# Kernel optimization log

Hardware: AMD Instinct MI355X
Metric: run time of the kernel (lower is better)

Reference implementation:

```python
import jax, jax.numpy as jnp
import numpy as np

B, L, D_MODEL, HEADS, EXP, DEPTH = 2, 2048, 1024, 16, 2, 12
D_EXP = D_MODEL * EXP
D_HEAD = D_EXP // HEADS


def _layernorm(x, g, b, eps=1e-5):
    mu = jnp.mean(x, axis=-1, keepdims=True)
    var = jnp.mean(jnp.square(x - mu), axis=-1, keepdims=True)
    return (x - mu) * jax.lax.rsqrt(var + eps) * g + b


def setup_inputs() -> dict:
    key = jax.random.key(0)
    ks = jax.random.split(key, 4)
    x = jax.random.normal(ks[0], (B, L, D_MODEL), dtype=jnp.float32)
    w_in = jax.random.normal(ks[1], (D_MODEL, 4 * D_EXP), dtype=jnp.float32) * 0.02
    w_out = jax.random.normal(ks[2], (D_EXP, D_MODEL), dtype=jnp.float32) * (0.02 / np.sqrt(2 * DEPTH))
    return {
        "x": x,
        "ln1_g": jnp.ones((D_MODEL,), jnp.float32),
        "ln1_b": jnp.zeros((D_MODEL,), jnp.float32),
        "ln2_g": jnp.ones((D_MODEL,), jnp.float32),
        "ln2_b": jnp.zeros((D_MODEL,), jnp.float32),
        "w_in": w_in,
        "w_out": w_out,
        "smear_factor": jnp.linspace(-6.0, 6.0, HEADS, dtype=jnp.float32),
        "log_scale": jnp.zeros((HEADS,), jnp.float32),
    }


def reference(x, ln1_g, ln1_b, ln2_g, ln2_b, w_in, w_out, smear_factor, log_scale):
    b, l, d = x.shape
    h = smear_factor.shape[0]
    d_exp = w_in.shape[1] // 4
    dh = d_exp // h

    qkvp = _layernorm(x, ln1_g, ln1_b) @ w_in  # [b, l, 4*d_exp]
    q, k, v, p = jnp.split(qkvp, 4, axis=-1)
    # 'b i (h d) -> b h i d'
    to_heads = lambda t: t.reshape(b, l, h, dh).transpose(0, 2, 1, 3)
    q, k, v = to_heads(q), to_heads(k), to_heads(v)

    # smeared keys: k_i <- (1-s)*k_i + s*k_{i-1}  (zero at i=0)
    smear = jax.nn.sigmoid(smear_factor)[None, :, None, None]
    k_prev = jnp.pad(k, ((0, 0), (0, 0), (1, 0), (0, 0)))[:, :, :-1, :]
    k = (1.0 - smear) * k + smear * k_prev

    # ALiBi-style additive mask: slope[h]*j on causal part, -1e10 above diag
    half = h // 2
    slopes = jnp.concatenate([2.0 ** jnp.linspace(0.0, -8.0, half), jnp.zeros((h - half,), jnp.float32)])
    j = jnp.arange(l)
    causal = jnp.where(j[None, :] > j[:, None], jnp.float32(-1e10), jnp.float32(0.0))  # [l, l]
    mask = slopes[:, None, None] * j[None, None, :].astype(jnp.float32) + causal[None, :, :]  # [h, l, l]

    # SDPA with q/s, k/s and default scale 1/sqrt(dh): logits = q k^T / (s^2 sqrt(dh))
    inv = 1.0 / (jnp.exp(2.0 * log_scale)[None, :, None, None] * jnp.sqrt(jnp.float32(dh)))
    logits = jnp.einsum('bhid,bhjd->bhij', q, k) * inv + mask[None]
    attn = jax.nn.softmax(logits, axis=-1)
    o = jnp.einsum('bhij,bhjd->bhid', attn, v)
    o = o.transpose(0, 2, 1, 3).reshape(b, l, h * dh)  # 'b h i d -> b i (h d)'

    out = (jax.nn.silu(p) * o) @ w_out
    return _layernorm(out, ln2_g, ln2_b)
```

## Files before the change

kernel.cpp:

```cpp
#include <hip/hip_runtime.h>

typedef unsigned short u16;
typedef __attribute__((ext_vector_type(8))) short bf16x8;
typedef __attribute__((ext_vector_type(8))) unsigned short u16x8;
typedef __attribute__((ext_vector_type(4))) float f32x4;

#define L_SEQ 2048
#define NTOK 4096
#define DMODEL 1024
#define DEXP 2048
#define NH 16
#define DH 128

__device__ __forceinline__ u16 f2bf(float f) {
    unsigned u = __float_as_uint(f);
    unsigned r = (u + 0x7FFFu + ((u >> 16) & 1u)) >> 16;
    return (u16)r;
}
__device__ __forceinline__ float bf2f(u16 h) {
    return __uint_as_float(((unsigned)h) << 16);
}

template <int CTRL>
__device__ __forceinline__ float dpp_f(float x) {
    return __int_as_float(__builtin_amdgcn_update_dpp(0, __float_as_int(x), CTRL, 0xF, 0xF, true));
}
__device__ __forceinline__ float red16_max(float x) {
    x = fmaxf(x, dpp_f<0xB1>(x));
    x = fmaxf(x, dpp_f<0x4E>(x));
    x = fmaxf(x, dpp_f<0x124>(x));
    x = fmaxf(x, dpp_f<0x128>(x));
    return x;
}
__device__ __forceinline__ float red16_sum(float x) {
    x += dpp_f<0xB1>(x);
    x += dpp_f<0x4E>(x);
    x += dpp_f<0x124>(x);
    x += dpp_f<0x128>(x);
    return x;
}

__device__ __forceinline__ void gl_lds16(const u16* g, u16* l) {
    __builtin_amdgcn_global_load_lds((const __attribute__((address_space(1))) void*)g,
                                     (__attribute__((address_space(3))) void*)l, 16, 0, 0);
}

__global__ void conv_transpose(const float* __restrict__ in, u16* __restrict__ out, int R, int C) {
    __shared__ unsigned tile[32][33];
    int c0 = blockIdx.x * 32, r0 = blockIdx.y * 32;
    int tx = threadIdx.x, ty = threadIdx.y;
    for (int j = 0; j < 32; j += 8)
        tile[ty + j][tx] = (unsigned)f2bf(in[(size_t)(r0 + ty + j) * C + c0 + tx]);
    __syncthreads();
    for (int j = 0; j < 32; j += 8)
        out[(size_t)(c0 + ty + j) * R + r0 + tx] = (u16)tile[tx][ty + j];
}

__global__ __launch_bounds__(256) void ln_fwd(const float* __restrict__ x, const float* __restrict__ g,
                                              const float* __restrict__ bta, void* __restrict__ outp,
                                              int out_bf16) {
    int row = blockIdx.x;
    int t = threadIdx.x;
    const float* xr = x + (size_t)row * DMODEL;
    float4 xv = *(const float4*)&xr[t * 4];
    float s = xv.x + xv.y + xv.z + xv.w;
    float s2 = xv.x * xv.x + xv.y * xv.y + xv.z * xv.z + xv.w * xv.w;
    for (int off = 32; off >= 1; off >>= 1) {
        s += __shfl_xor(s, off);
        s2 += __shfl_xor(s2, off);
    }
    __shared__ float red[10];
    int w = t >> 6;
    if ((t & 63) == 0) { red[w] = s; red[4 + w] = s2; }
    __syncthreads();
    if (t == 0) {
        red[8] = red[0] + red[1] + red[2] + red[3];
        red[9] = red[4] + red[5] + red[6] + red[7];
    }
    __syncthreads();
    float mu = red[8] * (1.0f / DMODEL);
    float var = red[9] * (1.0f / DMODEL) - mu * mu;
    float rstd = rsqrtf(var + 1e-5f);
    float vals[4] = {xv.x, xv.y, xv.z, xv.w};
    for (int e = 0; e < 4; e++) {
        int c = t * 4 + e;
        float y = (vals[e] - mu) * rstd * g[c] + bta[c];
        if (out_bf16) ((u16*)outp)[(size_t)row * DMODEL + c] = f2bf(y);
        else          ((float*)outp)[(size_t)row * DMODEL + c] = y;
    }
}

__device__ __forceinline__ void store_out(u16* C, size_t idx, float v) { C[idx] = f2bf(v); }
__device__ __forceinline__ void store_out(float* C, size_t idx, float v) { C[idx] = v; }

template <typename OutT>
__global__ __launch_bounds__(256) void gemm_bt(const u16* __restrict__ A, const u16* __restrict__ BT,
                                               OutT* __restrict__ C, int M, int N, int K) {
    __shared__ u16 a_s[4096];
    __shared__ u16 b_s[4096];
    int tid = threadIdx.x;
    int m0 = blockIdx.y * 128, n0 = blockIdx.x * 128;
    int w = tid >> 6, lane = tid & 63, quad = lane >> 4, ln = lane & 15;
    int wr = (w >> 1) * 64, wc = (w & 1) * 64;
    f32x4 zero4 = {0.f, 0.f, 0.f, 0.f};
    f32x4 acc[4][4];
    for (int r = 0; r < 4; r++)
        for (int c = 0; c < 4; c++) acc[r][c] = zero4;

    int lrow = lane >> 2, lseg = (lane & 3) * 8;
    const u16* Ag0 = A + (size_t)(m0 + 32 * w + lrow) * K + lseg;
    const u16* Ag1 = Ag0 + (size_t)16 * K;
    const u16* Bg0 = BT + (size_t)(n0 + 32 * w + lrow) * K + lseg;
    const u16* Bg1 = Bg0 + (size_t)16 * K;
    u16* al0 = &a_s[(2 * w) * 512];
    u16* al1 = &a_s[(2 * w + 1) * 512];
    u16* bl0 = &b_s[(2 * w) * 512];
    u16* bl1 = &b_s[(2 * w + 1) * 512];

    for (int k0 = 0; k0 < K; k0 += 32) {
        __syncthreads();
        gl_lds16(Ag0 + k0, al0);
        gl_lds16(Ag1 + k0, al1);
        gl_lds16(Bg0 + k0, bl0);
        gl_lds16(Bg1 + k0, bl1);
        __syncthreads();
        bf16x8 af[4], bfr[4];
        for (int r = 0; r < 4; r++) af[r]  = *(const bf16x8*)&a_s[(wr + r * 16 + ln) * 32 + quad * 8];
        for (int c = 0; c < 4; c++) bfr[c] = *(const bf16x8*)&b_s[(wc + c * 16 + ln) * 32 + quad * 8];
        for (int r = 0; r < 4; r++)
            for (int c = 0; c < 4; c++)
                acc[r][c] = __builtin_amdgcn_mfma_f32_16x16x32_bf16(af[r], bfr[c], acc[r][c], 0, 0, 0);
    }
    for (int r = 0; r < 4; r++)
        for (int c = 0; c < 4; c++)
            for (int e = 0; e < 4; e++) {
                int row = m0 + wr + r * 16 + quad * 4 + e;
                int col = n0 + wc + c * 16 + ln;
                store_out(C, (size_t)row * N + col, acc[r][c][e]);
            }
}

__global__ __launch_bounds__(256) void smear_kernel(const u16* __restrict__ qkvp,
                                                    const float* __restrict__ smear_f,
                                                    u16* __restrict__ k_sm) {
    int gid = blockIdx.x * 256 + threadIdx.x;
    int base = gid * 8;
    int bl = base >> 11;
    int c = base & 2047;
    int h = c >> 7;
    int d = c & 127;
    int l = bl & (L_SEQ - 1);
    int bb = bl >> 11;
    float s = 1.0f / (1.0f + __expf(-smear_f[h]));
    u16x8 cur = *(const u16x8*)&qkvp[(size_t)bl * 8192 + 2048 + c];
    u16x8 prv = {0, 0, 0, 0, 0, 0, 0, 0};
    if (l > 0) prv = *(const u16x8*)&qkvp[(size_t)(bl - 1) * 8192 + 2048 + c];
    u16x8 outv;
    for (int u = 0; u < 8; u++) {
        float kc = bf2f(cur[u]);
        float kp = bf2f(prv[u]);
        outv[u] = f2bf((1.0f - s) * kc + s * kp);
    }
    *(u16x8*)&k_sm[(((size_t)(bb * 16 + h)) * L_SEQ + l) * DH + d] = outv;
}

__global__ void vT_kernel(const u16* __restrict__ qkvp, u16* __restrict__ v_t) {
    __shared__ unsigned tile[32][33];
    int l0 = blockIdx.x * 32, d0 = blockIdx.y * 32;
    int bh = blockIdx.z;
    int bb = bh >> 4, h = bh & 15;
    int tx = threadIdx.x, ty = threadIdx.y;
    size_t tokb = (size_t)bb * L_SEQ;
    for (int j = 0; j < 32; j += 8)
        tile[ty + j][tx] = (unsigned)qkvp[(tokb + l0 + ty + j) * 8192 + 4096 + h * DH + d0 + tx];
    __syncthreads();
    for (int j = 0; j < 32; j += 8)
        v_t[((size_t)bh * DH + d0 + ty + j) * L_SEQ + l0 + tx] = (u16)tile[tx][ty + j];
}

__global__ __launch_bounds__(256) void attn_kernel(const u16* __restrict__ qkvp,
                                                   const u16* __restrict__ k_sm,
                                                   const u16* __restrict__ v_t,
                                                   u16* __restrict__ ag2,
                                                   const float* __restrict__ log_scale) {
    __shared__ u16 k_s[8192];
    __shared__ u16 vt_s[8192];
    __shared__ u16 p_s[4608];
    int tid = threadIdx.x;
    int bh = blockIdx.y;
    int bb = bh >> 4, h = bh & 15;
    int w = tid >> 6, lane = tid & 63, quad = lane >> 4, ln = lane & 15;
    size_t tokb = (size_t)bb * L_SEQ;

    const float LOG2E = 1.44269504f;
    float inv = 1.0f / (__expf(2.0f * log_scale[h]) * sqrtf((float)DH));
    float scl = inv * LOG2E;
    float slope2 = ((h < 8) ? exp2f(-8.0f * (float)h / 7.0f) : 0.0f) * LOG2E;

    int lrow = lane >> 2, lseg8 = (lane & 3) * 8;
    f32x4 zero4 = {0.f, 0.f, 0.f, 0.f};
    u16* pw = &p_s[w * 1152];

    for (int sidx = 0; sidx < 2; sidx++) {
        int ib = sidx == 0 ? (31 - (int)blockIdx.x) : (int)blockIdx.x;
        int i0 = ib * 64;
        int si = i0 + w * 16;

        bf16x8 qf[4];
        for (int kt = 0; kt < 4; kt++)
            qf[kt] = *(const bf16x8*)&qkvp[(tokb + si + ln) * 8192 + h * DH + kt * 32 + quad * 8];

        float m_i[4], l_i[4];
        for (int r = 0; r < 4; r++) { m_i[r] = -1e30f; l_i[r] = 0.f; }
        f32x4 o_acc[8];
        for (int dt = 0; dt < 8; dt++) o_acc[dt] = zero4;

        const u16* kg[4];
        for (int g = 0; g < 4; g++)
            kg[g] = k_sm + ((size_t)bh * L_SEQ + g * 16 + lrow) * DH + w * 32 + lseg8;
        const u16* vg[4];
        u16* vl[4];
        for (int q = 0; q < 4; q++) {
            int c = w * 4 + q;
            int jt = c >> 3, dg = c & 7;
            vg[q] = v_t + ((size_t)bh * DH + dg * 16 + lrow) * L_SEQ + jt * 32 + lseg8;
            vl[q] = &vt_s[jt * 4096 + dg * 512];
        }

        for (int j0 = 0; j0 <= i0; j0 += 64) {
            __syncthreads();
            for (int g = 0; g < 4; g++) {
                gl_lds16(kg[g], &k_s[w * 2048 + g * 512]);
                kg[g] += 64 * DH;
            }
            for (int q = 0; q < 4; q++) {
                gl_lds16(vg[q], vl[q]);
                vg[q] += 64;
            }
            __syncthreads();

            f32x4 sc[4];
            for (int ct = 0; ct < 4; ct++) sc[ct] = zero4;
            for (int kt = 0; kt < 4; kt++)
                for (int ct = 0; ct < 4; ct++) {
                    bf16x8 bfr = *(const bf16x8*)&k_s[kt * 2048 + (ct * 16 + ln) * 32 + quad * 8];
                    sc[ct] = __builtin_amdgcn_mfma_f32_16x16x32_bf16(qf[kt], bfr, sc[ct], 0, 0, 0);
                }

            bool full = (j0 + 63 <= si);
            float s2[4][4];
            float aj0 = slope2 * (float)(j0 + ln);
            for (int ct = 0; ct < 4; ct++) {
                float ajv = aj0 + slope2 * (float)(16 * ct);
                int j = j0 + ct * 16 + ln;
                for (int r = 0; r < 4; r++) {
                    float v = fmaf(sc[ct][r], scl, ajv);
                    if (!full) {
                        int i = si + quad * 4 + r;
                        if (j > i) v = -3.0e38f;
                    }
                    s2[ct][r] = v;
                }
            }
            float mnew[4], alpha[4];
            for (int r = 0; r < 4; r++) {
                float mr = fmaxf(fmaxf(s2[0][r], s2[1][r]), fmaxf(s2[2][r], s2[3][r]));
                mr = red16_max(mr);
                mnew[r] = fmaxf(m_i[r], mr);
                alpha[r] = exp2f(m_i[r] - mnew[r]);
                m_i[r] = mnew[r];
            }
            float rs[4] = {0.f, 0.f, 0.f, 0.f};
            for (int ct = 0; ct < 4; ct++)
                for (int r = 0; r < 4; r++) {
                    float p = exp2f(s2[ct][r] - mnew[r]);
                    u16 pb = (u16)(__float_as_uint(p) >> 16);
                    pw[(quad * 4 + r) * 72 + ct * 16 + ln] = pb;
                    rs[r] += bf2f(pb);
                }
            for (int r = 0; r < 4; r++) {
                float s = red16_sum(rs[r]);
                l_i[r] = fmaf(alpha[r], l_i[r], s);
            }
            for (int dt = 0; dt < 8; dt++) {
                f32x4 o = o_acc[dt];
                for (int r = 0; r < 4; r++) o[r] *= alpha[r];
                o_acc[dt] = o;
            }
            asm volatile("s_waitcnt lgkmcnt(0)" ::: "memory");
            for (int ks = 0; ks < 2; ks++) {
                bf16x8 pa = *(const bf16x8*)&pw[ln * 72 + ks * 32 + quad * 8];
                for (int dt = 0; dt < 8; dt++) {
                    bf16x8 vf = *(const bf16x8*)&vt_s[ks * 4096 + (dt * 16 + ln) * 32 + quad * 8];
                    o_acc[dt] = __builtin_amdgcn_mfma_f32_16x16x32_bf16(pa, vf, o_acc[dt], 0, 0, 0);
                }
            }
        }

        float rinv[4];
        for (int r = 0; r < 4; r++) rinv[r] = __builtin_amdgcn_rcpf(l_i[r]);
        for (int dt = 0; dt < 8; dt++)
            for (int r = 0; r < 4; r++) {
                int i = si + quad * 4 + r;
                int dcol = dt * 16 + ln;
                float o = o_acc[dt][r] * rinv[r];
                float pv = bf2f(qkvp[(tokb + i) * 8192 + 6144 + h * DH + dcol]);
                float gate = pv * __builtin_amdgcn_rcpf(1.0f + exp2f(-pv * LOG2E));
                ag2[(tokb + i) * 2048 + h * DH + dcol] = f2bf(gate * o);
            }
    }
}

extern "C" void kernel_launch(void* const* d_in, const int* in_sizes, int n_in,
                              void* d_out, int out_size, void* d_ws, size_t ws_size,
                              hipStream_t stream) {
    const float* x       = (const float*)d_in[0];
    const float* ln1_g   = (const float*)d_in[1];
    const float* ln1_b   = (const float*)d_in[2];
    const float* ln2_g   = (const float*)d_in[3];
    const float* ln2_b   = (const float*)d_in[4];
    const float* w_in    = (const float*)d_in[5];
    const float* w_out   = (const float*)d_in[6];
    const float* smear_f = (const float*)d_in[7];
    const float* logsc   = (const float*)d_in[8];
    float* out = (float*)d_out;
    char* ws = (char*)d_ws;

    u16* w_inT   = (u16*)(ws + 0);
    u16* w_outT  = (u16*)(ws + (size_t)16777216);
    u16* lnA     = (u16*)(ws + (size_t)20971520);
    u16* qkvp    = (u16*)(ws + (size_t)29360128);
    u16* k_sm    = (u16*)(ws + (size_t)96468992);
    u16* ag2     = (u16*)(ws + (size_t)113246208);
    float* out_pre = (float*)(ws + (size_t)96468992);
    u16* v_t     = (u16*)(ws + 0);

    dim3 b32x8(32, 8);
    conv_transpose<<<dim3(8192 / 32, 1024 / 32), b32x8, 0, stream>>>(w_in, w_inT, 1024, 8192);
    conv_transpose<<<dim3(1024 / 32, 2048 / 32), b32x8, 0, stream>>>(w_out, w_outT, 2048, 1024);
    ln_fwd<<<NTOK, 256, 0, stream>>>(x, ln1_g, ln1_b, (void*)lnA, 1);
    gemm_bt<u16><<<dim3(8192 / 128, 4096 / 128), 256, 0, stream>>>(lnA, w_inT, qkvp, NTOK, 8192, 1024);
    smear_kernel<<<4096, 256, 0, stream>>>(qkvp, smear_f, k_sm);
    vT_kernel<<<dim3(L_SEQ / 32, DH / 32, 32), b32x8, 0, stream>>>(qkvp, v_t);
    attn_kernel<<<dim3(16, 32), 256, 0, stream>>>(qkvp, k_sm, v_t, ag2, logsc);
    gemm_bt<float><<<dim3(1024 / 128, 4096 / 128), 256, 0, stream>>>(ag2, w_outT, out_pre, NTOK, 1024, 2048);
    ln_fwd<<<NTOK, 256, 0, stream>>>(out_pre, ln2_g, ln2_b, (void*)out, 0);
}
```

Baseline: 389.5 us.

## Enlarge attention query tile to 128 rows with MFMA row sums

Each attention block now handles one 128-row query tile, with each wave owning two 16-row m-tiles, so every K/V tile staged in LDS feeds twice as many MFMAs. This replaces the earlier scheme where each block processed two 64-row tiles paired for causal load balance. The softmax row sum is now accumulated with an MFMA against a ones vector instead of DPP reductions. Output rescaling is skipped when no row max changed, and launch bounds request two blocks per CU. The cost is that work per block is no longer balanced across the causal triangle, and register pressure rises from the doubled accumulators.

```diff
diff --git a/kernel.cpp b/kernel.cpp
--- a/kernel.cpp
+++ b/kernel.cpp
@@ -30,13 +30,6 @@
     x = fmaxf(x, dpp_f<0x4E>(x));
     x = fmaxf(x, dpp_f<0x124>(x));
     x = fmaxf(x, dpp_f<0x128>(x));
-    return x;
-}
-__device__ __forceinline__ float red16_sum(float x) {
-    x += dpp_f<0xB1>(x);
-    x += dpp_f<0x4E>(x);
-    x += dpp_f<0x124>(x);
-    x += dpp_f<0x128>(x);
     return x;
 }
 
@@ -178,132 +171,149 @@
         v_t[((size_t)bh * DH + d0 + ty + j) * L_SEQ + l0 + tx] = (u16)tile[tx][ty + j];
 }
 
-__global__ __launch_bounds__(256) void attn_kernel(const u16* __restrict__ qkvp,
-                                                   const u16* __restrict__ k_sm,
-                                                   const u16* __restrict__ v_t,
-                                                   u16* __restrict__ ag2,
-                                                   const float* __restrict__ log_scale) {
+__global__ __launch_bounds__(256, 2) void attn_kernel(const u16* __restrict__ qkvp,
+                                                      const u16* __restrict__ k_sm,
+                                                      const u16* __restrict__ v_t,
+                                                      u16* __restrict__ ag2,
+                                                      const float* __restrict__ log_scale) {
     __shared__ u16 k_s[8192];
     __shared__ u16 vt_s[8192];
-    __shared__ u16 p_s[4608];
+    __shared__ u16 p_s[9216];
     int tid = threadIdx.x;
+    int ib = 15 - (int)blockIdx.x;
+    int i0 = ib * 128;
     int bh = blockIdx.y;
     int bb = bh >> 4, h = bh & 15;
     int w = tid >> 6, lane = tid & 63, quad = lane >> 4, ln = lane & 15;
     size_t tokb = (size_t)bb * L_SEQ;
+    int si = i0 + w * 32;
 
     const float LOG2E = 1.44269504f;
     float inv = 1.0f / (__expf(2.0f * log_scale[h]) * sqrtf((float)DH));
     float scl = inv * LOG2E;
     float slope2 = ((h < 8) ? exp2f(-8.0f * (float)h / 7.0f) : 0.0f) * LOG2E;
 
+    bf16x8 qf[2][4];
+    for (int mt = 0; mt < 2; mt++)
+        for (int kt = 0; kt < 4; kt++)
+            qf[mt][kt] = *(const bf16x8*)&qkvp[(tokb + si + mt * 16 + ln) * 8192 + h * DH + kt * 32 + quad * 8];
+
+    float m_i[2][4];
+    for (int mt = 0; mt < 2; mt++)
+        for (int r = 0; r < 4; r++) m_i[mt][r] = -1e30f;
+    f32x4 zero4 = {0.f, 0.f, 0.f, 0.f};
+    f32x4 o_acc[2][8], l_acc[2];
+    for (int mt = 0; mt < 2; mt++) {
+        for (int dt = 0; dt < 8; dt++) o_acc[mt][dt] = zero4;
+        l_acc[mt] = zero4;
+    }
+    const short ONE_BF = (short)0x3F80;
+    bf16x8 ones = {ONE_BF, ONE_BF, ONE_BF, ONE_BF, ONE_BF, ONE_BF, ONE_BF, ONE_BF};
+
     int lrow = lane >> 2, lseg8 = (lane & 3) * 8;
-    f32x4 zero4 = {0.f, 0.f, 0.f, 0.f};
-    u16* pw = &p_s[w * 1152];
-
-    for (int sidx = 0; sidx < 2; sidx++) {
-        int ib = sidx == 0 ? (31 - (int)blockIdx.x) : (int)blockIdx.x;
-        int i0 = ib * 64;
-        int si = i0 + w * 16;
-
-        bf16x8 qf[4];
+    const u16* kg[4];
+    for (int g = 0; g < 4; g++)
+        kg[g] = k_sm + ((size_t)bh * L_SEQ + g * 16 + lrow) * DH + w * 32 + lseg8;
+    const u16* vg[4];
+    u16* vl[4];
+    for (int q = 0; q < 4; q++) {
+        int c = w * 4 + q;
+        int jt = c >> 3, dg = c & 7;
+        vg[q] = v_t + ((size_t)bh * DH + dg * 16 + lrow) * L_SEQ + jt * 32 + lseg8;
+        vl[q] = &vt_s[jt * 4096 + dg * 512];
+    }
+    u16* pw = &p_s[w * 2304];
+
+    for (int j0 = 0; j0 <= i0 + 64; j0 += 64) {
+        __syncthreads();
+        for (int g = 0; g < 4; g++) {
+            gl_lds16(kg[g], &k_s[w * 2048 + g * 512]);
+            kg[g] += 64 * DH;
+        }
+        for (int q = 0; q < 4; q++) {
+            gl_lds16(vg[q], vl[q]);
+            vg[q] += 64;
+        }
+        __syncthreads();
+        if (j0 > si + 31) continue;
+
+        f32x4 sc[2][4];
+        for (int mt = 0; mt < 2; mt++)
+            for (int ct = 0; ct < 4; ct++) sc[mt][ct] = zero4;
         for (int kt = 0; kt < 4; kt++)
-            qf[kt] = *(const bf16x8*)&qkvp[(tokb + si + ln) * 8192 + h * DH + kt * 32 + quad * 8];
-
-        float m_i[4], l_i[4];
-        for (int r = 0; r < 4; r++) { m_i[r] = -1e30f; l_i[r] = 0.f; }
-        f32x4 o_acc[8];
-        for (int dt = 0; dt < 8; dt++) o_acc[dt] = zero4;
-
-        const u16* kg[4];
-        for (int g = 0; g < 4; g++)
-            kg[g] = k_sm + ((size_t)bh * L_SEQ + g * 16 + lrow) * DH + w * 32 + lseg8;
-        const u16* vg[4];
-        u16* vl[4];
-        for (int q = 0; q < 4; q++) {
-            int c = w * 4 + q;
-            int jt = c >> 3, dg = c & 7;
-            vg[q] = v_t + ((size_t)bh * DH + dg * 16 + lrow) * L_SEQ + jt * 32 + lseg8;
-            vl[q] = &vt_s[jt * 4096 + dg * 512];
-        }
-
-        for (int j0 = 0; j0 <= i0; j0 += 64) {
-            __syncthreads();
-            for (int g = 0; g < 4; g++) {
-                gl_lds16(kg[g], &k_s[w * 2048 + g * 512]);
-                kg[g] += 64 * DH;
-            }
-            for (int q = 0; q < 4; q++) {
-                gl_lds16(vg[q], vl[q]);
-                vg[q] += 64;
-            }
-            __syncthreads();
-
-            f32x4 sc[4];
-            for (int ct = 0; ct < 4; ct++) sc[ct] = zero4;
-            for (int kt = 0; kt < 4; kt++)
-                for (int ct = 0; ct < 4; ct++) {
-                    bf16x8 bfr = *(const bf16x8*)&k_s[kt * 2048 + (ct * 16 + ln) * 32 + quad * 8];
-                    sc[ct] = __builtin_amdgcn_mfma_f32_16x16x32_bf16(qf[kt], bfr, sc[ct], 0, 0, 0);
-                }
-
-            bool full = (j0 + 63 <= si);
+            for (int ct = 0; ct < 4; ct++) {
+                bf16x8 bfr = *(const bf16x8*)&k_s[kt * 2048 + (ct * 16 + ln) * 32 + quad * 8];
+                sc[0][ct] = __builtin_amdgcn_mfma_f32_16x16x32_bf16(qf[0][kt], bfr, sc[0][ct], 0, 0, 0);
+                sc[1][ct] = __builtin_amdgcn_mfma_f32_16x16x32_bf16(qf[1][kt], bfr, sc[1][ct], 0, 0, 0);
+            }
+
+        float alpha[2][4];
+        bool any_resc = false;
+        float aj0 = slope2 * (float)(j0 + ln);
+        for (int mt = 0; mt < 2; mt++) {
+            int smt = si + mt * 16;
+            bool full = (j0 + 63 <= smt);
             float s2[4][4];
-            float aj0 = slope2 * (float)(j0 + ln);
             for (int ct = 0; ct < 4; ct++) {
                 float ajv = aj0 + slope2 * (float)(16 * ct);
                 int j = j0 + ct * 16 + ln;
                 for (int r = 0; r < 4; r++) {
-                    float v = fmaf(sc[ct][r], scl, ajv);
+                    float v = fmaf(sc[mt][ct][r], scl, ajv);
                     if (!full) {
-                        int i = si + quad * 4 + r;
+                        int i = smt + quad * 4 + r;
                         if (j > i) v = -3.0e38f;
                     }
                     s2[ct][r] = v;
                 }
             }
-            float mnew[4], alpha[4];
             for (int r = 0; r < 4; r++) {
                 float mr = fmaxf(fmaxf(s2[0][r], s2[1][r]), fmaxf(s2[2][r], s2[3][r]));
                 mr = red16_max(mr);
-                mnew[r] = fmaxf(m_i[r], mr);
-                alpha[r] = exp2f(m_i[r] - mnew[r]);
-                m_i[r] = mnew[r];
-            }
-            float rs[4] = {0.f, 0.f, 0.f, 0.f};
-            for (int ct = 0; ct < 4; ct++)
-                for (int r = 0; r < 4; r++) {
-                    float p = exp2f(s2[ct][r] - mnew[r]);
+                float mnew = fmaxf(m_i[mt][r], mr);
+                alpha[mt][r] = exp2f(m_i[mt][r] - mnew);
+                any_resc |= (alpha[mt][r] != 1.0f);
+                m_i[mt][r] = mnew;
+                for (int ct = 0; ct < 4; ct++) {
+                    float p = exp2f(s2[ct][r] - mnew);
                     u16 pb = (u16)(__float_as_uint(p) >> 16);
-                    pw[(quad * 4 + r) * 72 + ct * 16 + ln] = pb;
-                    rs[r] += bf2f(pb);
+                    pw[(mt * 16 + quad * 4 + r) * 72 + ct * 16 + ln] = pb;
                 }
-            for (int r = 0; r < 4; r++) {
-                float s = red16_sum(rs[r]);
-                l_i[r] = fmaf(alpha[r], l_i[r], s);
-            }
+            }
+        }
+        if (__any(any_resc)) {
+            for (int mt = 0; mt < 2; mt++) {
+                for (int dt = 0; dt < 8; dt++) {
+                    f32x4 o = o_acc[mt][dt];
+                    for (int r = 0; r < 4; r++) o[r] *= alpha[mt][r];
+                    o_acc[mt][dt] = o;
+                }
+                f32x4 lv = l_acc[mt];
+                for (int r = 0; r < 4; r++) lv[r] *= alpha[mt][r];
+                l_acc[mt] = lv;
+            }
+        }
+        asm volatile("s_waitcnt lgkmcnt(0)" ::: "memory");
+        for (int ks = 0; ks < 2; ks++) {
+            bf16x8 pa0 = *(const bf16x8*)&pw[ln * 72 + ks * 32 + quad * 8];
+            bf16x8 pa1 = *(const bf16x8*)&pw[(16 + ln) * 72 + ks * 32 + quad * 8];
+            l_acc[0] = __builtin_amdgcn_mfma_f32_16x16x32_bf16(pa0, ones, l_acc[0], 0, 0, 0);
+            l_acc[1] = __builtin_amdgcn_mfma_f32_16x16x32_bf16(pa1, ones, l_acc[1], 0, 0, 0);
             for (int dt = 0; dt < 8; dt++) {
-                f32x4 o = o_acc[dt];
-                for (int r = 0; r < 4; r++) o[r] *= alpha[r];
-                o_acc[dt] = o;
-            }
-            asm volatile("s_waitcnt lgkmcnt(0)" ::: "memory");
-            for (int ks = 0; ks < 2; ks++) {
-                bf16x8 pa = *(const bf16x8*)&pw[ln * 72 + ks * 32 + quad * 8];
-                for (int dt = 0; dt < 8; dt++) {
-                    bf16x8 vf = *(const bf16x8*)&vt_s[ks * 4096 + (dt * 16 + ln) * 32 + quad * 8];
-                    o_acc[dt] = __builtin_amdgcn_mfma_f32_16x16x32_bf16(pa, vf, o_acc[dt], 0, 0, 0);
-                }
-            }
-        }
-
+                bf16x8 vf = *(const bf16x8*)&vt_s[ks * 4096 + (dt * 16 + ln) * 32 + quad * 8];
+                o_acc[0][dt] = __builtin_amdgcn_mfma_f32_16x16x32_bf16(pa0, vf, o_acc[0][dt], 0, 0, 0);
+                o_acc[1][dt] = __builtin_amdgcn_mfma_f32_16x16x32_bf16(pa1, vf, o_acc[1][dt], 0, 0, 0);
+            }
+        }
+    }
+
+    for (int mt = 0; mt < 2; mt++) {
         float rinv[4];
-        for (int r = 0; r < 4; r++) rinv[r] = __builtin_amdgcn_rcpf(l_i[r]);
+        for (int r = 0; r < 4; r++) rinv[r] = __builtin_amdgcn_rcpf(l_acc[mt][r]);
         for (int dt = 0; dt < 8; dt++)
             for (int r = 0; r < 4; r++) {
-                int i = si + quad * 4 + r;
+                int i = si + mt * 16 + quad * 4 + r;
                 int dcol = dt * 16 + ln;
-                float o = o_acc[dt][r] * rinv[r];
+                float o = o_acc[mt][dt][r] * rinv[r];
                 float pv = bf2f(qkvp[(tokb + i) * 8192 + 6144 + h * DH + dcol]);
                 float gate = pv * __builtin_amdgcn_rcpf(1.0f + exp2f(-pv * LOG2E));
                 ag2[(tokb + i) * 2048 + h * DH + dcol] = f2bf(gate * o);
```

Result: slower. 413.4 us (+6.1%).

## Compute softmax row sums via MFMA with ones, skip masked tiles and rescales

Applied to the files above, without the earlier changes.

The per-row softmax denominator is no longer built from scalar adds plus DPP cross-lane reductions. It is accumulated with an extra MFMA that multiplies the P tile by a ones vector, using the bf16-rounded P values. Warps whose 16 rows lie entirely before the current key tile now skip score and PV work after the shared loads. The O and l rescale by alpha is skipped when no lane's running max changed. These changes cut VALU and cross-lane work in the attention inner loop, at the cost of one more MFMA per k-step and a wave-wide vote.

```diff
diff --git a/kernel.cpp b/kernel.cpp
--- a/kernel.cpp
+++ b/kernel.cpp
@@ -30,13 +30,6 @@
     x = fmaxf(x, dpp_f<0x4E>(x));
     x = fmaxf(x, dpp_f<0x124>(x));
     x = fmaxf(x, dpp_f<0x128>(x));
-    return x;
-}
-__device__ __forceinline__ float red16_sum(float x) {
-    x += dpp_f<0xB1>(x);
-    x += dpp_f<0x4E>(x);
-    x += dpp_f<0x124>(x);
-    x += dpp_f<0x128>(x);
     return x;
 }
 
@@ -200,6 +193,8 @@
     int lrow = lane >> 2, lseg8 = (lane & 3) * 8;
     f32x4 zero4 = {0.f, 0.f, 0.f, 0.f};
     u16* pw = &p_s[w * 1152];
+    const short ONE_BF = (short)0x3F80;
+    bf16x8 ones = {ONE_BF, ONE_BF, ONE_BF, ONE_BF, ONE_BF, ONE_BF, ONE_BF, ONE_BF};
 
     for (int sidx = 0; sidx < 2; sidx++) {
         int ib = sidx == 0 ? (31 - (int)blockIdx.x) : (int)blockIdx.x;
@@ -210,10 +205,11 @@
         for (int kt = 0; kt < 4; kt++)
             qf[kt] = *(const bf16x8*)&qkvp[(tokb + si + ln) * 8192 + h * DH + kt * 32 + quad * 8];
 
-        float m_i[4], l_i[4];
-        for (int r = 0; r < 4; r++) { m_i[r] = -1e30f; l_i[r] = 0.f; }
-        f32x4 o_acc[8];
+        float m_i[4];
+        for (int r = 0; r < 4; r++) m_i[r] = -1e30f;
+        f32x4 o_acc[8], l_acc;
         for (int dt = 0; dt < 8; dt++) o_acc[dt] = zero4;
+        l_acc = zero4;
 
         const u16* kg[4];
         for (int g = 0; g < 4; g++)
@@ -238,6 +234,7 @@
                 vg[q] += 64;
             }
             __syncthreads();
+            if (j0 > si + 15) continue;
 
             f32x4 sc[4];
             for (int ct = 0; ct < 4; ct++) sc[ct] = zero4;
@@ -262,34 +259,33 @@
                     s2[ct][r] = v;
                 }
             }
-            float mnew[4], alpha[4];
+            float alpha[4];
+            bool any_resc = false;
             for (int r = 0; r < 4; r++) {
                 float mr = fmaxf(fmaxf(s2[0][r], s2[1][r]), fmaxf(s2[2][r], s2[3][r]));
                 mr = red16_max(mr);
-                mnew[r] = fmaxf(m_i[r], mr);
-                alpha[r] = exp2f(m_i[r] - mnew[r]);
-                m_i[r] = mnew[r];
-            }
-            float rs[4] = {0.f, 0.f, 0.f, 0.f};
-            for (int ct = 0; ct < 4; ct++)
-                for (int r = 0; r < 4; r++) {
-                    float p = exp2f(s2[ct][r] - mnew[r]);
+                float mnew = fmaxf(m_i[r], mr);
+                alpha[r] = exp2f(m_i[r] - mnew);
+                any_resc |= (alpha[r] != 1.0f);
+                m_i[r] = mnew;
+                for (int ct = 0; ct < 4; ct++) {
+                    float p = exp2f(s2[ct][r] - mnew);
                     u16 pb = (u16)(__float_as_uint(p) >> 16);
                     pw[(quad * 4 + r) * 72 + ct * 16 + ln] = pb;
-                    rs[r] += bf2f(pb);
-                }
-            for (int r = 0; r < 4; r++) {
-                float s = red16_sum(rs[r]);
-                l_i[r] = fmaf(alpha[r], l_i[r], s);
-            }
-            for (int dt = 0; dt < 8; dt++) {
-                f32x4 o = o_acc[dt];
-                for (int r = 0; r < 4; r++) o[r] *= alpha[r];
-                o_acc[dt] = o;
+                }
+            }
+            if (__any(any_resc)) {
+                for (int dt = 0; dt < 8; dt++) {
+                    f32x4 o = o_acc[dt];
+                    for (int r = 0; r < 4; r++) o[r] *= alpha[r];
+                    o_acc[dt] = o;
+                }
+                for (int r = 0; r < 4; r++) l_acc[r] *= alpha[r];
             }
             asm volatile("s_waitcnt lgkmcnt(0)" ::: "memory");
             for (int ks = 0; ks < 2; ks++) {
                 bf16x8 pa = *(const bf16x8*)&pw[ln * 72 + ks * 32 + quad * 8];
+                l_acc = __builtin_amdgcn_mfma_f32_16x16x32_bf16(pa, ones, l_acc, 0, 0, 0);
                 for (int dt = 0; dt < 8; dt++) {
                     bf16x8 vf = *(const bf16x8*)&vt_s[ks * 4096 + (dt * 16 + ln) * 32 + quad * 8];
                     o_acc[dt] = __builtin_amdgcn_mfma_f32_16x16x32_bf16(pa, vf, o_acc[dt], 0, 0, 0);
@@ -298,7 +294,7 @@
         }
 
         float rinv[4];
-        for (int r = 0; r < 4; r++) rinv[r] = __builtin_amdgcn_rcpf(l_i[r]);
+        for (int r = 0; r < 4; r++) rinv[r] = __builtin_amdgcn_rcpf(l_acc[r]);
         for (int dt = 0; dt < 8; dt++)
             for (int r = 0; r < 4; r++) {
                 int i = si + quad * 4 + r;
```

New measurement: 383.9 us. About the same (-1.5%).
